# Kernel optimization log

Hardware: AMD Instinct MI355X
Metric: run time of the kernel (lower is better)

## Reference

```python
import jax
import jax.numpy as jnp
import numpy as np

# ---- static config (mirrors ReduceMask.__init__ / get_block_params) ----
N, H, W = 32, 1024, 1024
BH, BW = 16, 16            # block_size (pool window)
KH, KW = 3, 3              # kernel_size
SH, SW = 1, 1              # stride
PH, PW = KH // 2, KW // 2  # symmetric padding = 1,1
BSH, BSW = BH - KH + SH, BW - KW + SW   # block_stride = 14,14
BCH = (H + 2 * PH - BH) // BSH + 1      # block_cnt h = 73
BCW = (W + 2 * PW - BW) // BSW + 1      # block_cnt w = 73
THRESHOLD = 0.9
TOTAL = N * BCH * BCW      # fixed upper bound on number of active blocks


def setup_inputs() -> dict:
    key = jax.random.key(0)
    mask = jax.random.uniform(key, (N, 1, H, W), dtype=jnp.float32)
    return {"mask": mask}


def reference(mask):
    # pad H,W by kernel_size//2 (constant zeros), as in F.pad(mask, padding)
    x = jnp.pad(mask, ((0, 0), (0, 0), (PH, PH), (PW, PW)))
    # max_pool2d with window=block_size, stride=block_stride, padding=0
    pooled = jax.lax.reduce_window(
        x, -jnp.inf, jax.lax.max,
        window_dimensions=(1, 1, BH, BW),
        window_strides=(1, 1, BSH, BSW),
        padding='VALID',
    )[:, 0]  # squeeze channel -> [N, BCH, BCW]
    active = pooled > THRESHOLD
    # torch.nonzero -> row-major (n, bh, bw) indices; fixed-size padded with -1 for jit
    nz = jnp.nonzero(active, size=TOTAL, fill_value=-1)
    return jnp.stack(nz, axis=1).astype(jnp.int32)  # [TOTAL, 3]
```

## Files before the change

### kernel.cpp

```cpp
#include <hip/hip_runtime.h>

#define NI    32
#define HH    1024
#define WW    1024
#define BHW   16
#define BS    14
#define NBH   73
#define NBW   73
#define NCHUNK (NI * NBH)
#define TOTAL  (NI * NBH * NBW)

struct umask2 { unsigned long long x, y; };

__device__ __forceinline__ float4 max4(float4 a, float4 b) {
    return make_float4(fmaxf(a.x, b.x), fmaxf(a.y, b.y),
                       fmaxf(a.z, b.z), fmaxf(a.w, b.w));
}

__global__ __launch_bounds__(256, 4) void pool_kernel(const float* __restrict__ mask,
                                                      umask2* __restrict__ masks,
                                                      int* __restrict__ counts) {
    const int chunk = blockIdx.x;
    const int n  = chunk / NBH;
    const int by = chunk % NBH;
    const int tid  = threadIdx.x;
    const int lane = tid & 63;
    const int wave = tid >> 6;

    __shared__ float colmax[WW];
    __shared__ unsigned long long wb[4];
    __shared__ int sdone[4];
    __shared__ unsigned long long sm0, sm1;

    const int r0 = by * BS - 1;
    const int rs = max(r0, 0);
    const int nr = (by > 0) ? 16 : 15;
    const float* p = mask + (size_t)n * HH * WW + (size_t)rs * WW + tid * 4;

    float4 m = make_float4(-1e30f, -1e30f, -1e30f, -1e30f);
    bool done = false;

    for (int k = 0; k < 8 && !done; ++k) {
        const int r1 = 2 * k, r2 = 2 * k + 1;
        m = max4(m, *(const float4*)(p + (size_t)r1 * WW));
        if (r2 < nr)
            m = max4(m, *(const float4*)(p + (size_t)r2 * WW));

        const float mm = fmaxf(fmaxf(m.x, m.y), fmaxf(m.z, m.w));
        const unsigned long long bal = __ballot(mm > 0.9f);
        if (lane == 0) wb[wave] = bal;
        __syncthreads();

        bool whit = true;
        if (tid < NBW) {
            const int c0 = tid * BS;
            const int lo = (c0 + 2) >> 2;
            const int hi = (c0 + 11) >> 2;
            const int w0 = lo >> 6, sh = lo & 63;
            unsigned long long bits = wb[w0] >> sh;
            if (w0 < 3 && sh) bits |= wb[w0 + 1] << (64 - sh);
            const int nb = hi - lo + 1;
            whit = (bits & ((1ull << nb) - 1ull)) != 0ull;
        }
        const unsigned long long miss = __ballot(!whit);
        if (lane == 0) sdone[wave] = (miss == 0ull);
        __syncthreads();
        done = (sdone[0] & sdone[1] & sdone[2] & sdone[3]) != 0;
        __syncthreads();
    }

    if (done) {
        if (tid == 0) {
            umask2 mmk; mmk.x = ~0ull; mmk.y = (1ull << (NBW - 64)) - 1ull;
            masks[chunk] = mmk;
            counts[chunk] = NBW;
        }
        return;
    }

    const int c = tid * 4;
    colmax[c + 0] = m.x;
    colmax[c + 1] = m.y;
    colmax[c + 2] = m.z;
    colmax[c + 3] = m.w;
    __syncthreads();

    int f = 0;
    if (tid < NBW) {
        const int c0 = tid * BS - 1;
        float mx = colmax[max(c0, 0)];
        #pragma unroll
        for (int dc = 1; dc < BHW; ++dc) mx = fmaxf(mx, colmax[c0 + dc]);
        f = (mx > 0.9f) ? 1 : 0;
    }
    const unsigned long long b = __ballot(f);
    if (wave == 0 && lane == 0) sm0 = b;
    if (wave == 1 && lane == 0) sm1 = b;
    __syncthreads();
    if (tid == 0) {
        umask2 mm2; mm2.x = sm0; mm2.y = sm1;
        masks[chunk] = mm2;
        counts[chunk] = __popcll(sm0) + __popcll(sm1);
    }
}

__global__ __launch_bounds__(128) void scatter_kernel(const umask2* __restrict__ masks,
                                                      const int* __restrict__ counts,
                                                      int* __restrict__ out) {
    const int chunk = blockIdx.x;
    const int n  = chunk / NBH;
    const int by = chunk % NBH;
    const int tid  = threadIdx.x;
    const int lane = tid & 63;
    const int wave = tid >> 6;

    __shared__ int wsum[2];

    int partial = 0;
    for (int i = tid; i < chunk; i += 128) partial += counts[i];
    #pragma unroll
    for (int off = 32; off > 0; off >>= 1) partial += __shfl_down(partial, off, 64);
    if (lane == 0) wsum[wave] = partial;

    const umask2 m = masks[chunk];
    __syncthreads();
    const int e = wsum[0] + wsum[1];
    const int c = __popcll(m.x) + __popcll(m.y);

    if (tid < NBW) {
        int f, prefix;
        if (wave == 0) {
            f = (int)((m.x >> tid) & 1ull);
            prefix = __popcll(m.x & ((1ull << tid) - 1ull));
        } else {
            const int t = tid - 64;
            f = (int)((m.y >> t) & 1ull);
            prefix = __popcll(m.x) + __popcll(m.y & ((1ull << t) - 1ull));
        }
        if (f) {
            const int pos = e + prefix;
            out[3 * pos + 0] = n;
            out[3 * pos + 1] = by;
            out[3 * pos + 2] = tid;
        }
    }

    const int slack = NBW - c;
    if (slack > 0) {
        const int s_incl = (chunk + 1) * NBW - (e + c);
        const int base3 = 3 * (TOTAL - s_incl);
        const int n3 = 3 * slack;
        for (int i = tid; i < n3; i += 128) out[base3 + i] = -1;
    }
}

extern "C" void kernel_launch(void* const* d_in, const int* in_sizes, int n_in,
                              void* d_out, int out_size, void* d_ws, size_t ws_size,
                              hipStream_t stream) {
    const float* mask = (const float*)d_in[0];
    int* out = (int*)d_out;

    umask2* masks = (umask2*)d_ws;
    int* counts = (int*)(masks + NCHUNK);

    pool_kernel<<<NCHUNK, 256, 0, stream>>>(mask, masks, counts);
    scatter_kernel<<<NCHUNK, 128, 0, stream>>>(masks, counts, out);
}
```

Measured before the change: 177.1 us.

## Write full-row output in pool kernel and skip scatter when all chunks full

The pool kernel now loads the first six rows unconditionally and does a single early-exit check with __syncthreads_and, instead of an iterative check after every two rows. Chunks where all 73 blocks are active write their output rows directly, and any chunk that is not full increments a global deficit counter. The scatter kernel returns immediately when the deficit is zero, which skips the prefix-sum work in the common dense case. This adds a memset launch and an atomic, and a partially-hit chunk now always reads six rows before it can decide.

```diff
diff --git a/kernel.cpp b/kernel.cpp
--- a/kernel.cpp
+++ b/kernel.cpp
@@ -9,6 +9,7 @@
 #define NBW   73
 #define NCHUNK (NI * NBH)
 #define TOTAL  (NI * NBH * NBW)
+#define ROWDW  (3 * NBW)
 
 struct umask2 { unsigned long long x, y; };
 
@@ -17,9 +18,20 @@
                        fmaxf(a.z, b.z), fmaxf(a.w, b.w));
 }
 
-__global__ __launch_bounds__(256, 4) void pool_kernel(const float* __restrict__ mask,
+__device__ __forceinline__ void write_full_row(int* __restrict__ out,
+                                               int chunk, int n, int by, int tid) {
+    if (tid < ROWDW) {
+        const int q = tid / 3;
+        const int comp = tid - 3 * q;
+        out[(size_t)chunk * ROWDW + tid] = (comp == 0) ? n : ((comp == 1) ? by : q);
+    }
+}
+
+__global__ __launch_bounds__(256, 8) void pool_kernel(const float* __restrict__ mask,
                                                       umask2* __restrict__ masks,
-                                                      int* __restrict__ counts) {
+                                                      int* __restrict__ counts,
+                                                      int* __restrict__ deficit,
+                                                      int* __restrict__ out) {
     const int chunk = blockIdx.x;
     const int n  = chunk / NBH;
     const int by = chunk % NBH;
@@ -29,7 +41,6 @@
 
     __shared__ float colmax[WW];
     __shared__ unsigned long long wb[4];
-    __shared__ int sdone[4];
     __shared__ unsigned long long sm0, sm1;
 
     const int r0 = by * BS - 1;
@@ -37,46 +48,44 @@
     const int nr = (by > 0) ? 16 : 15;
     const float* p = mask + (size_t)n * HH * WW + (size_t)rs * WW + tid * 4;
 
-    float4 m = make_float4(-1e30f, -1e30f, -1e30f, -1e30f);
-    bool done = false;
+    const float4 a0 = *(const float4*)(p + 0 * (size_t)WW);
+    const float4 a1 = *(const float4*)(p + 1 * (size_t)WW);
+    const float4 a2 = *(const float4*)(p + 2 * (size_t)WW);
+    const float4 a3 = *(const float4*)(p + 3 * (size_t)WW);
+    const float4 a4 = *(const float4*)(p + 4 * (size_t)WW);
+    const float4 a5 = *(const float4*)(p + 5 * (size_t)WW);
+    float4 m = max4(max4(max4(a0, a1), max4(a2, a3)), max4(a4, a5));
 
-    for (int k = 0; k < 8 && !done; ++k) {
-        const int r1 = 2 * k, r2 = 2 * k + 1;
-        m = max4(m, *(const float4*)(p + (size_t)r1 * WW));
-        if (r2 < nr)
-            m = max4(m, *(const float4*)(p + (size_t)r2 * WW));
+    const float mm = fmaxf(fmaxf(m.x, m.y), fmaxf(m.z, m.w));
+    const unsigned long long bal = __ballot(mm > 0.9f);
+    if (lane == 0) wb[wave] = bal;
+    __syncthreads();
 
-        const float mm = fmaxf(fmaxf(m.x, m.y), fmaxf(m.z, m.w));
-        const unsigned long long bal = __ballot(mm > 0.9f);
-        if (lane == 0) wb[wave] = bal;
-        __syncthreads();
-
-        bool whit = true;
-        if (tid < NBW) {
-            const int c0 = tid * BS;
-            const int lo = (c0 + 2) >> 2;
-            const int hi = (c0 + 11) >> 2;
-            const int w0 = lo >> 6, sh = lo & 63;
-            unsigned long long bits = wb[w0] >> sh;
-            if (w0 < 3 && sh) bits |= wb[w0 + 1] << (64 - sh);
-            const int nb = hi - lo + 1;
-            whit = (bits & ((1ull << nb) - 1ull)) != 0ull;
-        }
-        const unsigned long long miss = __ballot(!whit);
-        if (lane == 0) sdone[wave] = (miss == 0ull);
-        __syncthreads();
-        done = (sdone[0] & sdone[1] & sdone[2] & sdone[3]) != 0;
-        __syncthreads();
+    bool whit = true;
+    if (tid < NBW) {
+        const int c0 = tid * BS;
+        const int lo = (c0 + 2) >> 2;
+        const int hi = (c0 + 11) >> 2;
+        const int w0 = lo >> 6, sh = lo & 63;
+        unsigned long long bits = wb[w0] >> sh;
+        if (w0 < 3 && sh) bits |= wb[w0 + 1] << (64 - sh);
+        const int nb = hi - lo + 1;
+        whit = (bits & ((1ull << nb) - 1ull)) != 0ull;
     }
+    const bool done = __syncthreads_and((int)whit) != 0;
 
     if (done) {
         if (tid == 0) {
-            umask2 mmk; mmk.x = ~0ull; mmk.y = (1ull << (NBW - 64)) - 1ull;
-            masks[chunk] = mmk;
+            umask2 mk; mk.x = ~0ull; mk.y = (1ull << (NBW - 64)) - 1ull;
+            masks[chunk] = mk;
             counts[chunk] = NBW;
         }
+        write_full_row(out, chunk, n, by, tid);
         return;
     }
+
+    for (int r = 6; r < nr; ++r)
+        m = max4(m, *(const float4*)(p + (size_t)r * WW));
 
     const int c = tid * 4;
     colmax[c + 0] = m.x;
@@ -97,16 +106,24 @@
     if (wave == 0 && lane == 0) sm0 = b;
     if (wave == 1 && lane == 0) sm1 = b;
     __syncthreads();
+
+    const int cnt = __popcll(sm0) + __popcll(sm1);
     if (tid == 0) {
-        umask2 mm2; mm2.x = sm0; mm2.y = sm1;
-        masks[chunk] = mm2;
-        counts[chunk] = __popcll(sm0) + __popcll(sm1);
+        umask2 mk; mk.x = sm0; mk.y = sm1;
+        masks[chunk] = mk;
+        counts[chunk] = cnt;
+        if (cnt != NBW) atomicAdd(deficit, 1);
     }
+    if (cnt == NBW)
+        write_full_row(out, chunk, n, by, tid);
 }
 
 __global__ __launch_bounds__(128) void scatter_kernel(const umask2* __restrict__ masks,
                                                       const int* __restrict__ counts,
+                                                      const int* __restrict__ deficit,
                                                       int* __restrict__ out) {
+    if (*deficit == 0) return;
+
     const int chunk = blockIdx.x;
     const int n  = chunk / NBH;
     const int by = chunk % NBH;
@@ -162,7 +179,9 @@
 
     umask2* masks = (umask2*)d_ws;
     int* counts = (int*)(masks + NCHUNK);
+    int* deficit = counts + NCHUNK;
 
-    pool_kernel<<<NCHUNK, 256, 0, stream>>>(mask, masks, counts);
-    scatter_kernel<<<NCHUNK, 128, 0, stream>>>(masks, counts, out);
+    hipMemsetAsync(deficit, 0, sizeof(int), stream);
+    pool_kernel<<<NCHUNK, 256, 0, stream>>>(mask, masks, counts, deficit, out);
+    scatter_kernel<<<NCHUNK, 128, 0, stream>>>(masks, counts, deficit, out);
 }
```

New measurement: 179.9 us. Within noise of the previous version (+1.6%).
